# Kernel tuning notes

Measured on AMD Instinct MI355X. Metric: run time of the kernel, lower is better.

## Reference

```python
import jax, jax.numpy as jnp
import numpy as np

N_NODES = 50000
N_EDGES = 800000
IN_DIM, HID_DIM, OUT_DIM = 128, 128, 64


def setup_inputs() -> dict:
    key = jax.random.key(0)
    ks = jax.random.split(key, 8)
    x = jax.random.normal(ks[0], (N_NODES, IN_DIM), dtype=jnp.float32)
    edge_index = jax.random.randint(ks[1], (2, N_EDGES), 0, N_NODES, dtype=jnp.int64)
    # GCNConv uses Glorot weights + zero bias; any random init is fine for a reference
    W1 = jax.random.normal(ks[2], (IN_DIM, HID_DIM), dtype=jnp.float32) / np.sqrt(IN_DIM)
    b1 = jnp.zeros((HID_DIM,), dtype=jnp.float32)
    W2 = jax.random.normal(ks[3], (HID_DIM, OUT_DIM), dtype=jnp.float32) / np.sqrt(HID_DIM)
    b2 = jnp.zeros((OUT_DIM,), dtype=jnp.float32)
    Wfc = jax.random.normal(ks[4], (OUT_DIM, 2), dtype=jnp.float32) / np.sqrt(OUT_DIM)
    bfc = jnp.zeros((2,), dtype=jnp.float32)
    return {"x": x, "edge_index": edge_index, "W1": W1, "b1": b1,
            "W2": W2, "b2": b2, "Wfc": Wfc, "bfc": bfc}


def _gcn_conv(x, src, dst, W, b, n_nodes):
    """PyG GCNConv: out = D^{-1/2} (A+I) D^{-1/2} (x W) + b."""
    xw = x @ W  # [N, F_out] transform before propagation
    ones = jnp.ones(src.shape[0], dtype=xw.dtype)
    deg = jax.ops.segment_sum(ones, dst, num_segments=n_nodes) + 1.0  # +1 for self-loop
    dinv = jax.lax.rsqrt(deg)
    norm = dinv[src] * dinv[dst]  # [E]
    msg = xw[src] * norm[:, None]  # gather + scale: [E, F_out]
    agg = jax.ops.segment_sum(msg, dst, num_segments=n_nodes)  # scatter-add
    agg = agg + xw * (dinv * dinv)[:, None]  # self-loop contribution (norm = 1/deg)
    return agg + b


def reference(x, edge_index, W1, b1, W2, b2, Wfc, bfc):
    n = x.shape[0]
    src, dst = edge_index[0], edge_index[1]
    h = jax.nn.relu(_gcn_conv(x, src, dst, W1, b1, n))
    # dropout is identity in eval mode
    h = _gcn_conv(h, src, dst, W2, b2, n)
    h = h @ Wfc + bfc
    return jax.nn.leaky_relu(h, negative_slope=0.01)
```

## Files before the change

### kernel.cpp

```cpp
#include <hip/hip_runtime.h>
#include <hip/hip_fp16.h>

#define IN_DIM 128
#define HID_DIM 128
#define OUT_DIM 64
#define BINW 128
#define BINSHIFT 7
#define MAXBIN 512
#define CAP 4096
#define CNTSTRIDE 16
#define SC_GRID 256

__global__ __launch_bounds__(256) void k_build_gemm(const float* __restrict__ x,
                                                    const float* __restrict__ W,
                                                    __half* __restrict__ xwh,
                                                    const int* __restrict__ src,
                                                    const int* __restrict__ dst,
                                                    int* __restrict__ bin_cnt,
                                                    int* __restrict__ ovf_cnt,
                                                    unsigned int* __restrict__ ovf,
                                                    unsigned int* __restrict__ ebin,
                                                    int N, int E, int nbin) {
    __shared__ union SMem {
        float Ws[64][128];
        struct { int h[MAXBIN]; int base_s[MAXBIN]; } sc;
    } smem;
    const int nGemm = (N + 127) >> 7;
    int tid = threadIdx.x;

    if ((int)blockIdx.x < nGemm) {
        float4* Ws4 = (float4*)&smem.Ws[0][0];
        int tx = tid & 15, ty = tid >> 4;
        int row0 = blockIdx.x * 128;
        int rows[8];
        const float* xr[8];
#pragma unroll
        for (int j = 0; j < 8; ++j) {
            int row = row0 + ty + 16 * j;
            rows[j] = row;
            if (row > N - 1) row = N - 1;
            xr[j] = x + (size_t)row * IN_DIM;
        }
        float4 aclo[8], achi[8];
#pragma unroll
        for (int j = 0; j < 8; ++j) {
            aclo[j] = make_float4(0.f, 0.f, 0.f, 0.f);
            achi[j] = make_float4(0.f, 0.f, 0.f, 0.f);
        }
#pragma unroll
        for (int ph = 0; ph < 2; ++ph) {
            const float4* W4 = (const float4*)(W + (size_t)ph * 64 * HID_DIM);
#pragma unroll
            for (int i = 0; i < 8; ++i) Ws4[tid + 256 * i] = W4[tid + 256 * i];
            __syncthreads();
#pragma unroll 2
            for (int k4 = 0; k4 < 16; ++k4) {
                float4 av[8];
#pragma unroll
                for (int j = 0; j < 8; ++j) av[j] = *(const float4*)(xr[j] + ph * 64 + k4 * 4);
#pragma unroll
                for (int kk = 0; kk < 4; ++kk) {
                    float4 blo = *(const float4*)&smem.Ws[k4 * 4 + kk][4 * tx];
                    float4 bhi = *(const float4*)&smem.Ws[k4 * 4 + kk][64 + 4 * tx];
#pragma unroll
                    for (int j = 0; j < 8; ++j) {
                        float a = (kk == 0) ? av[j].x : (kk == 1) ? av[j].y : (kk == 2) ? av[j].z : av[j].w;
                        aclo[j].x += a * blo.x; aclo[j].y += a * blo.y;
                        aclo[j].z += a * blo.z; aclo[j].w += a * blo.w;
                        achi[j].x += a * bhi.x; achi[j].y += a * bhi.y;
                        achi[j].z += a * bhi.z; achi[j].w += a * bhi.w;
                    }
                }
            }
            __syncthreads();
        }
#pragma unroll
        for (int j = 0; j < 8; ++j) {
            if (rows[j] < N) {
                union { __half2 h[2]; uint2 u; } lo, hi;
                lo.h[0] = __floats2half2_rn(aclo[j].x, aclo[j].y);
                lo.h[1] = __floats2half2_rn(aclo[j].z, aclo[j].w);
                hi.h[0] = __floats2half2_rn(achi[j].x, achi[j].y);
                hi.h[1] = __floats2half2_rn(achi[j].z, achi[j].w);
                uint2* p = (uint2*)(xwh + (size_t)rows[j] * HID_DIM);
                p[tx] = lo.u;
                p[16 + tx] = hi.u;
            }
        }
    } else {
        int sb = blockIdx.x - nGemm;
        int* h = smem.sc.h;
        int* base_s = smem.sc.base_s;
        for (int k = tid; k < nbin; k += 256) h[k] = 0;
        __syncthreads();
        int per = E / SC_GRID;
        int ebeg = sb * per;
        int eend = (sb + 1 == SC_GRID) ? E : ebeg + per;
        for (int i = ebeg + tid; i < eend; i += 256)
            atomicAdd(&h[dst[i] >> BINSHIFT], 1);
        __syncthreads();
        for (int k = tid; k < nbin; k += 256) {
            int c = h[k];
            base_s[k] = (c > 0) ? atomicAdd(&bin_cnt[k * CNTSTRIDE], c) : 0;
            h[k] = 0;
        }
        __syncthreads();
        for (int i = ebeg + tid; i < eend; i += 256) {
            unsigned int s = (unsigned int)src[i];
            unsigned int d = (unsigned int)dst[i];
            int b = (int)(d >> BINSHIFT);
            int pos = base_s[b] + atomicAdd(&h[b], 1);
            unsigned int packed = s | (d << 16);
            if (pos < CAP) ebin[(size_t)b * CAP + pos] = packed;
            else ovf[atomicAdd(ovf_cnt, 1)] = packed;
        }
    }
}

__global__ __launch_bounds__(256) void k_fill(const unsigned int* __restrict__ ebin,
                                              const int* __restrict__ bin_cnt,
                                              const int* __restrict__ ovf_cnt,
                                              const unsigned int* __restrict__ ovf,
                                              int* __restrict__ row_ptr,
                                              unsigned short* __restrict__ degu,
                                              unsigned short* __restrict__ csr_src,
                                              float* __restrict__ dinv,
                                              const float* __restrict__ W2,
                                              const float* __restrict__ Wfc,
                                              const float* __restrict__ b2,
                                              const float* __restrict__ bfc,
                                              float* __restrict__ Wc,
                                              float* __restrict__ bc,
                                              int N, int nbin) {
    __shared__ int cnt[BINW];
    __shared__ int excl[BINW];
    __shared__ int start[BINW];
    int k = blockIdx.x;
    int node0 = k * BINW;
    int nn = min(BINW, N - node0);
    int t = threadIdx.x;
    if (t < BINW) cnt[t] = 0;
    __syncthreads();
    int cnt_k = min(bin_cnt[k * CNTSTRIDE], CAP);
    const unsigned int* seg = ebin + (size_t)k * CAP;
    for (int i = t; i < cnt_k; i += 256)
        atomicAdd(&cnt[(seg[i] >> 16) & (BINW - 1)], 1);
    int novf = *ovf_cnt;
    for (int i = t; i < novf; i += 256) {
        unsigned int e = ovf[i];
        if ((int)(e >> (16 + BINSHIFT)) == k)
            atomicAdd(&cnt[(e >> 16) & (BINW - 1)], 1);
    }
    __syncthreads();
    if (t < BINW) excl[t] = (t < nn) ? cnt[t] : 0;
    __syncthreads();
    for (int off = 1; off < BINW; off <<= 1) {
        int u = 0;
        if (t < BINW && t >= off) u = excl[t - off];
        __syncthreads();
        if (t < BINW) excl[t] += u;
        __syncthreads();
    }
    if (t < nn) {
        int deg = cnt[t];
        int e0 = k * CAP + excl[t] - deg;
        start[t] = e0;
        row_ptr[node0 + t] = e0;
        degu[node0 + t] = (unsigned short)deg;
        dinv[node0 + t] = rsqrtf((float)deg + 1.0f);
        cnt[t] = 0;
    }
    __syncthreads();
    for (int i = t; i < cnt_k; i += 256) {
        unsigned int e = seg[i];
        int dl = (e >> 16) & (BINW - 1);
        int slot = start[dl] + atomicAdd(&cnt[dl], 1);
        csr_src[slot] = (unsigned short)(e & 0xffffu);
    }
    for (int i = t; i < novf; i += 256) {
        unsigned int e = ovf[i];
        if ((int)(e >> (16 + BINSHIFT)) == k) {
            int dl = (e >> 16) & (BINW - 1);
            int slot = start[dl] + atomicAdd(&cnt[dl], 1);
            csr_src[slot] = (unsigned short)(e & 0xffffu);
        }
    }
    if (k == 0) {
        int kk = t >> 1, j = t & 1;
        float acc = 0.f;
#pragma unroll 8
        for (int m = 0; m < OUT_DIM; ++m) acc += W2[kk * OUT_DIM + m] * Wfc[m * 2 + j];
        Wc[kk * 2 + j] = acc;
        if (kk == 0) {
            float b = 0.f;
#pragma unroll 8
            for (int m = 0; m < OUT_DIM; ++m) b += b2[m] * Wfc[m * 2 + j];
            bc[j] = b + bfc[j];
        }
    }
}

__global__ __launch_bounds__(256) void k_agg1z(const int* __restrict__ row_ptr,
                                               const unsigned short* __restrict__ degu,
                                               const unsigned short* __restrict__ csr_src,
                                               const float* __restrict__ dinv,
                                               const __half* __restrict__ xwh,
                                               const float* __restrict__ b1,
                                               const float* __restrict__ Wc,
                                               float* __restrict__ z, int N) {
    constexpr int F = HID_DIM;
    constexpr int L = F / 8;
    constexpr int EPW = 64 / L;
    __shared__ float Wcs[HID_DIM * 2];
    int tid = threadIdx.x;
    if (tid < 64) ((float4*)Wcs)[tid] = ((const float4*)Wc)[tid];
    __syncthreads();
    int node = (blockIdx.x * 256 + tid) >> 6;
    if (node >= N) return;
    int lane = tid & 63;
    int sub = lane / L;
    int c   = lane % L;
    int beg = row_ptr[node];
    int end = beg + degu[node];
    float dd = dinv[node];
    uint4 us = *(const uint4*)(xwh + (size_t)node * F + c * 8);
    float4 b1a = *(const float4*)(b1 + c * 8);
    float4 b1b = *(const float4*)(b1 + c * 8 + 4);
    float a0 = 0.f, a1 = 0.f, a2 = 0.f, a3 = 0.f;
    float a4 = 0.f, a5 = 0.f, a6 = 0.f, a7 = 0.f;
    auto acc = [&](uint4 u, float w) {
        float2 v0 = __half22float2(*(__half2*)&u.x);
        float2 v1 = __half22float2(*(__half2*)&u.y);
        float2 v2 = __half22float2(*(__half2*)&u.z);
        float2 v3 = __half22float2(*(__half2*)&u.w);
        a0 = fmaf(v0.x, w, a0); a1 = fmaf(v0.y, w, a1);
        a2 = fmaf(v1.x, w, a2); a3 = fmaf(v1.y, w, a3);
        a4 = fmaf(v2.x, w, a4); a5 = fmaf(v2.y, w, a5);
        a6 = fmaf(v3.x, w, a6); a7 = fmaf(v3.y, w, a7);
    };
    int j = beg + sub;
    for (; j + 3 * EPW < end; j += 4 * EPW) {
        int s0 = csr_src[j];
        int s1 = csr_src[j + EPW];
        int s2 = csr_src[j + 2 * EPW];
        int s3 = csr_src[j + 3 * EPW];
        uint4 u0 = *(const uint4*)(xwh + (size_t)s0 * F + c * 8);
        uint4 u1 = *(const uint4*)(xwh + (size_t)s1 * F + c * 8);
        uint4 u2 = *(const uint4*)(xwh + (size_t)s2 * F + c * 8);
        uint4 u3 = *(const uint4*)(xwh + (size_t)s3 * F + c * 8);
        float w0 = dinv[s0];
        float w1 = dinv[s1];
        float w2 = dinv[s2];
        float w3 = dinv[s3];
        acc(u0, w0); acc(u1, w1); acc(u2, w2); acc(u3, w3);
    }
    for (; j < end; j += EPW) {
        int s = csr_src[j];
        uint4 u = *(const uint4*)(xwh + (size_t)s * F + c * 8);
        acc(u, dinv[s]);
    }
#pragma unroll
    for (int off = L; off < 64; off <<= 1) {
        a0 += __shfl_xor(a0, off); a1 += __shfl_xor(a1, off);
        a2 += __shfl_xor(a2, off); a3 += __shfl_xor(a3, off);
        a4 += __shfl_xor(a4, off); a5 += __shfl_xor(a5, off);
        a6 += __shfl_xor(a6, off); a7 += __shfl_xor(a7, off);
    }
    float2 v0 = __half22float2(*(__half2*)&us.x);
    float2 v1 = __half22float2(*(__half2*)&us.y);
    float2 v2 = __half22float2(*(__half2*)&us.z);
    float2 v3 = __half22float2(*(__half2*)&us.w);
    float h[8];
    h[0] = fmaxf(fmaf(fmaf(v0.x, dd, a0), dd, b1a.x), 0.f);
    h[1] = fmaxf(fmaf(fmaf(v0.y, dd, a1), dd, b1a.y), 0.f);
    h[2] = fmaxf(fmaf(fmaf(v1.x, dd, a2), dd, b1a.z), 0.f);
    h[3] = fmaxf(fmaf(fmaf(v1.y, dd, a3), dd, b1a.w), 0.f);
    h[4] = fmaxf(fmaf(fmaf(v2.x, dd, a4), dd, b1b.x), 0.f);
    h[5] = fmaxf(fmaf(fmaf(v2.y, dd, a5), dd, b1b.y), 0.f);
    h[6] = fmaxf(fmaf(fmaf(v3.x, dd, a6), dd, b1b.z), 0.f);
    h[7] = fmaxf(fmaf(fmaf(v3.y, dd, a7), dd, b1b.w), 0.f);
    float o0 = 0.f, o1 = 0.f;
#pragma unroll
    for (int k = 0; k < 8; ++k) {
        o0 += h[k] * Wcs[(c * 8 + k) * 2 + 0];
        o1 += h[k] * Wcs[(c * 8 + k) * 2 + 1];
    }
#pragma unroll
    for (int off = 1; off < L; off <<= 1) {
        o0 += __shfl_xor(o0, off);
        o1 += __shfl_xor(o1, off);
    }
    if (lane == 0) {
        float2 r; r.x = o0 * dd; r.y = o1 * dd;
        *(float2*)(z + (size_t)node * 2) = r;
    }
}

__global__ __launch_bounds__(256) void k_agg2(const int* __restrict__ row_ptr,
                                              const unsigned short* __restrict__ degu,
                                              const unsigned short* __restrict__ csr_src,
                                              const float* __restrict__ dinv,
                                              const float* __restrict__ z,
                                              const float* __restrict__ bc,
                                              float* __restrict__ out, int N) {
    int tid = threadIdx.x;
    int gwave = (blockIdx.x * 256 + tid) >> 6;
    int lane = tid & 63;
    int grp = lane >> 3, li = lane & 7;
    int node = gwave * 8 + grp;
    if (node >= N) return;
    int beg = row_ptr[node];
    int end = beg + degu[node];
    float s0 = 0.f, s1 = 0.f;
    int j = beg + li;
    for (; j + 8 < end; j += 16) {
        int sa = csr_src[j];
        int sb = csr_src[j + 8];
        float2 za = *(const float2*)(z + (size_t)sa * 2);
        float2 zb = *(const float2*)(z + (size_t)sb * 2);
        s0 += za.x + zb.x; s1 += za.y + zb.y;
    }
    if (j < end) {
        int s = csr_src[j];
        float2 zv = *(const float2*)(z + (size_t)s * 2);
        s0 += zv.x; s1 += zv.y;
    }
#pragma unroll
    for (int off = 1; off < 8; off <<= 1) {
        s0 += __shfl_xor(s0, off);
        s1 += __shfl_xor(s1, off);
    }
    if (li == 0) {
        float2 zs = *(const float2*)(z + (size_t)node * 2);
        float dd = dinv[node];
        float o0 = (s0 + zs.x) * dd + bc[0];
        float o1 = (s1 + zs.y) * dd + bc[1];
        float2 r;
        r.x = o0 > 0.f ? o0 : 0.01f * o0;
        r.y = o1 > 0.f ? o1 : 0.01f * o1;
        *(float2*)(out + (size_t)node * 2) = r;
    }
}

extern "C" void kernel_launch(void* const* d_in, const int* in_sizes, int n_in,
                              void* d_out, int out_size, void* d_ws, size_t ws_size,
                              hipStream_t stream) {
    const float* x   = (const float*)d_in[0];
    const int*   ei  = (const int*)d_in[1];
    const float* W1  = (const float*)d_in[2];
    const float* b1  = (const float*)d_in[3];
    const float* W2  = (const float*)d_in[4];
    const float* b2  = (const float*)d_in[5];
    const float* Wfc = (const float*)d_in[6];
    const float* bfc = (const float*)d_in[7];

    const int N = in_sizes[0] / IN_DIM;
    const int E = in_sizes[1] / 2;
    const int* src = ei;
    const int* dst = ei + E;
    const int nbin = (N + BINW - 1) / BINW;

    char* base = (char*)d_ws;
    size_t off = 0;
    auto take = [&](size_t bytes) { size_t o = off; off = (off + bytes + 255) & ~(size_t)255; return (void*)(base + o); };
    int*    row_ptr  = (int*)take((size_t)N * 4);
    unsigned short* degu = (unsigned short*)take((size_t)N * 2);
    unsigned short* csr_src = (unsigned short*)take((size_t)nbin * CAP * 2);
    int*    bin_cnt  = (int*)take((size_t)(nbin * CNTSTRIDE + CNTSTRIDE) * 4);
    int*    ovf_cnt  = bin_cnt + nbin * CNTSTRIDE;
    unsigned int* ovf = (unsigned int*)take((size_t)E * 4);
    unsigned int* ebin = (unsigned int*)take((size_t)nbin * CAP * 4);
    float*  dinv     = (float*)take((size_t)N * 4);
    __half* xw1h     = (__half*)take((size_t)N * HID_DIM * 2);
    float*  zbuf     = (float*)take((size_t)N * 2 * 4);
    float*  Wc       = (float*)take((size_t)HID_DIM * 2 * 4);
    float*  bc       = (float*)take(2 * 4);

    hipMemsetAsync(bin_cnt, 0, (size_t)(nbin * CNTSTRIDE + CNTSTRIDE) * 4, stream);

    const int nGemm = (N + 127) / 128;
    k_build_gemm<<<nGemm + SC_GRID, 256, 0, stream>>>(x, W1, xw1h, src, dst, bin_cnt,
                                                      ovf_cnt, ovf, ebin, N, E, nbin);
    k_fill<<<nbin, 256, 0, stream>>>(ebin, bin_cnt, ovf_cnt, ovf, row_ptr, degu,
                                     csr_src, dinv, W2, Wfc, b2, bfc, Wc, bc, N, nbin);
    k_agg1z<<<(N + 3) / 4, 256, 0, stream>>>(row_ptr, degu, csr_src, dinv, xw1h, b1, Wc, zbuf, N);
    const int nAgg2 = ((N + 7) / 8 * 64 + 255) / 256;
    k_agg2<<<nAgg2, 256, 0, stream>>>(row_ptr, degu, csr_src, dinv, zbuf, bc, (float*)d_out, N);
}
```

Before: 164.7 us.

## Use MFMA f16 matrix cores with hi/lo split for first-layer GEMM

Replaces the scalar FP32 FMA tiling for x@W1 with MFMA 16x16x32 f16 instructions. W is converted once to fp16 into a swizzled LDS layout to avoid bank conflicts. x is split into high and low fp16 parts so the products keep near-fp32 accuracy, which doubles the MFMA count. This moves the GEMM onto the matrix cores, but the weights are now rounded to fp16, which slightly changes precision.

```diff
diff --git a/kernel.cpp b/kernel.cpp
--- a/kernel.cpp
+++ b/kernel.cpp
@@ -10,6 +10,9 @@
 #define CAP 4096
 #define CNTSTRIDE 16
 #define SC_GRID 256
+
+typedef _Float16 f16x8 __attribute__((ext_vector_type(8)));
+typedef float f32x4 __attribute__((ext_vector_type(4)));
 
 __global__ __launch_bounds__(256) void k_build_gemm(const float* __restrict__ x,
                                                     const float* __restrict__ W,
@@ -22,69 +25,100 @@
                                                     unsigned int* __restrict__ ebin,
                                                     int N, int E, int nbin) {
     __shared__ union SMem {
-        float Ws[64][128];
+        unsigned int wt_raw[8192];
         struct { int h[MAXBIN]; int base_s[MAXBIN]; } sc;
     } smem;
     const int nGemm = (N + 127) >> 7;
     int tid = threadIdx.x;
 
     if ((int)blockIdx.x < nGemm) {
-        float4* Ws4 = (float4*)&smem.Ws[0][0];
-        int tx = tid & 15, ty = tid >> 4;
-        int row0 = blockIdx.x * 128;
-        int rows[8];
-        const float* xr[8];
-#pragma unroll
-        for (int j = 0; j < 8; ++j) {
-            int row = row0 + ty + 16 * j;
-            rows[j] = row;
-            if (row > N - 1) row = N - 1;
-            xr[j] = x + (size_t)row * IN_DIM;
-        }
-        float4 aclo[8], achi[8];
-#pragma unroll
-        for (int j = 0; j < 8; ++j) {
-            aclo[j] = make_float4(0.f, 0.f, 0.f, 0.f);
-            achi[j] = make_float4(0.f, 0.f, 0.f, 0.f);
-        }
-#pragma unroll
-        for (int ph = 0; ph < 2; ++ph) {
-            const float4* W4 = (const float4*)(W + (size_t)ph * 64 * HID_DIM);
-#pragma unroll
-            for (int i = 0; i < 8; ++i) Ws4[tid + 256 * i] = W4[tid + 256 * i];
-            __syncthreads();
-#pragma unroll 2
-            for (int k4 = 0; k4 < 16; ++k4) {
-                float4 av[8];
-#pragma unroll
-                for (int j = 0; j < 8; ++j) av[j] = *(const float4*)(xr[j] + ph * 64 + k4 * 4);
-#pragma unroll
-                for (int kk = 0; kk < 4; ++kk) {
-                    float4 blo = *(const float4*)&smem.Ws[k4 * 4 + kk][4 * tx];
-                    float4 bhi = *(const float4*)&smem.Ws[k4 * 4 + kk][64 + 4 * tx];
-#pragma unroll
-                    for (int j = 0; j < 8; ++j) {
-                        float a = (kk == 0) ? av[j].x : (kk == 1) ? av[j].y : (kk == 2) ? av[j].z : av[j].w;
-                        aclo[j].x += a * blo.x; aclo[j].y += a * blo.y;
-                        aclo[j].z += a * blo.z; aclo[j].w += a * blo.w;
-                        achi[j].x += a * bhi.x; achi[j].y += a * bhi.y;
-                        achi[j].z += a * bhi.z; achi[j].w += a * bhi.w;
-                    }
+        char* wb = (char*)smem.wt_raw;
+        {
+            int kk0 = (tid & 15) * 2;
+            int c8  = (tid >> 4) * 8;
+#pragma unroll
+            for (int i = 0; i < 4; ++i) {
+                int kk = i * 32 + kk0;
+                const float* w0 = W + (size_t)kk * HID_DIM + c8;
+                const float* w1 = w0 + HID_DIM;
+                float4 a0 = *(const float4*)w0;
+                float4 a1 = *(const float4*)(w0 + 4);
+                float4 b0 = *(const float4*)w1;
+                float4 b1 = *(const float4*)(w1 + 4);
+                float va[8] = {a0.x, a0.y, a0.z, a0.w, a1.x, a1.y, a1.z, a1.w};
+                float vb[8] = {b0.x, b0.y, b0.z, b0.w, b1.x, b1.y, b1.z, b1.w};
+#pragma unroll
+                for (int j = 0; j < 8; ++j) {
+                    int col = c8 + j;
+                    int byte = (col << 8) + (kk << 1);
+                    byte ^= ((col & 7) << 4);
+                    *(__half2*)(wb + byte) = __floats2half2_rn(va[j], vb[j]);
                 }
             }
-            __syncthreads();
-        }
-#pragma unroll
-        for (int j = 0; j < 8; ++j) {
-            if (rows[j] < N) {
-                union { __half2 h[2]; uint2 u; } lo, hi;
-                lo.h[0] = __floats2half2_rn(aclo[j].x, aclo[j].y);
-                lo.h[1] = __floats2half2_rn(aclo[j].z, aclo[j].w);
-                hi.h[0] = __floats2half2_rn(achi[j].x, achi[j].y);
-                hi.h[1] = __floats2half2_rn(achi[j].z, achi[j].w);
-                uint2* p = (uint2*)(xwh + (size_t)rows[j] * HID_DIM);
-                p[tx] = lo.u;
-                p[16 + tx] = hi.u;
+        }
+        int lane = tid & 63;
+        int wv   = tid >> 6;
+        int lcol = lane & 15;
+        int lk   = (lane >> 4) << 3;
+        int swz  = (lcol & 7) << 4;
+        int rb   = blockIdx.x * 128 + wv * 32;
+        int rows[2];
+        const float* xp[2];
+#pragma unroll
+        for (int r = 0; r < 2; ++r) {
+            int row = rb + 16 * r + lcol;
+            rows[r] = row;
+            if (row > N - 1) row = N - 1;
+            xp[r] = x + (size_t)row * IN_DIM + lk;
+        }
+        f32x4 acc[2][8];
+#pragma unroll
+        for (int r = 0; r < 2; ++r)
+#pragma unroll
+            for (int c = 0; c < 8; ++c) acc[r][c] = (f32x4){0.f, 0.f, 0.f, 0.f};
+
+        __syncthreads();
+
+        auto mk = [](float4 f0, float4 f1, f16x8& hi, f16x8& lo) {
+            float f[8] = {f0.x, f0.y, f0.z, f0.w, f1.x, f1.y, f1.z, f1.w};
+#pragma unroll
+            for (int e = 0; e < 8; ++e) {
+                _Float16 h = (_Float16)f[e];
+                hi[e] = h;
+                lo[e] = (_Float16)(f[e] - (float)h);
+            }
+        };
+#pragma unroll
+        for (int kc = 0; kc < 4; ++kc) {
+            f16x8 xhi[2], xlo[2];
+#pragma unroll
+            for (int r = 0; r < 2; ++r) {
+                float4 f0 = *(const float4*)(xp[r] + kc * 32);
+                float4 f1 = *(const float4*)(xp[r] + kc * 32 + 4);
+                mk(f0, f1, xhi[r], xlo[r]);
+            }
+#pragma unroll
+            for (int c = 0; c < 8; ++c) {
+                int ad = ((c << 12) | (lcol << 8) | ((kc << 6) + (lk << 1))) ^ swz;
+                f16x8 wfrag = *(const f16x8*)(wb + ad);
+                acc[0][c] = __builtin_amdgcn_mfma_f32_16x16x32_f16(wfrag, xhi[0], acc[0][c], 0, 0, 0);
+                acc[0][c] = __builtin_amdgcn_mfma_f32_16x16x32_f16(wfrag, xlo[0], acc[0][c], 0, 0, 0);
+                acc[1][c] = __builtin_amdgcn_mfma_f32_16x16x32_f16(wfrag, xhi[1], acc[1][c], 0, 0, 0);
+                acc[1][c] = __builtin_amdgcn_mfma_f32_16x16x32_f16(wfrag, xlo[1], acc[1][c], 0, 0, 0);
+            }
+        }
+        int cq = lane >> 4;
+#pragma unroll
+        for (int r = 0; r < 2; ++r) {
+            if (rows[r] < N) {
+                uint2* p = (uint2*)(xwh + (size_t)rows[r] * HID_DIM);
+#pragma unroll
+                for (int c = 0; c < 8; ++c) {
+                    union { __half2 h[2]; uint2 u; } pk;
+                    pk.h[0] = __floats2half2_rn(acc[r][c].x, acc[r][c].y);
+                    pk.h[1] = __floats2half2_rn(acc[r][c].z, acc[r][c].w);
+                    p[4 * c + cq] = pk.u;
+                }
             }
         }
     } else {
```

Result: faster. 156.0 us (-5.3%).
